# Optimization experiments

Hardware: AMD Instinct MI355X
Metric: run time of the kernel (lower is better)

## Reference

```python
import jax, jax.numpy as jnp
import numpy as np


def setup_inputs() -> dict:
    key = jax.random.key(0)
    k1, k2 = jax.random.split(key)
    B, S, D, T = 64, 1024, 512, 2048
    x = jax.random.normal(k1, (B, S, D), dtype=jnp.float32)
    durations = jax.random.randint(k2, (B, S), 0, 8, dtype=jnp.int32)
    return {"x": x, "durations": durations, "max_length": T}


def reference(x, durations, max_length):
    # x: [B, S, D]; durations: [B, S] (non-negative ints); max_length: static int.
    # Equivalent to per-sample repeat_interleave + pad_sequence + slice to max_length,
    # assuming max(sum(durations, axis=1)) >= max_length (true by construction here,
    # matching torch's min(lengths.max(), max_length) == max_length).
    S = x.shape[1]
    cum = jnp.cumsum(durations, axis=1)          # [B, S] exclusive boundary cumsum
    t = jnp.arange(max_length)                   # [T]
    # idx[b, t] = source phoneme index producing output frame t
    idx = jax.vmap(lambda c: jnp.searchsorted(c, t, side='right'))(cum)  # [B, T]
    lengths = cum[:, -1]                         # [B] total frames per sample
    mask = t[None, :] >= lengths[:, None]        # [B, T] True = padding (matches torch ~(<))
    idx = jnp.minimum(idx, S - 1)                # clip out-of-range indices (masked anyway)
    out = jnp.take_along_axis(x, idx[:, :, None], axis=1)  # [B, T, D] gather
    out = jnp.where(mask[:, :, None], jnp.zeros((), x.dtype), out)  # pad value 0
    return out, mask
```

## Files before the change

kernel.cpp:

```cpp
#include <hip/hip_runtime.h>

constexpr int B = 64;
constexpr int S = 1024;
constexpr int D = 512;
constexpr int T = 2048;
constexpr int FPB = 64;
constexpr int CHUNKS = T / FPB;

typedef float floatx4 __attribute__((ext_vector_type(4)));

__global__ __launch_bounds__(256) void lr_scan_kernel(
    const int* __restrict__ dur,
    int*       __restrict__ fidx,
    float*     __restrict__ mask)
{
    __shared__ int cum[S];
    __shared__ int wave_tot[4];

    const int tid  = threadIdx.x;
    const int b    = blockIdx.x;
    const int lane = tid & 63;
    const int wv   = tid >> 6;

    const int4 d4 = ((const int4*)(dur + b * S))[tid];
    const int p0 = d4.x;
    const int p1 = p0 + d4.y;
    const int p2 = p1 + d4.z;
    const int p3 = p2 + d4.w;

    int incl = p3;
    #pragma unroll
    for (int off = 1; off < 64; off <<= 1) {
        const int v = __shfl_up(incl, off, 64);
        if (lane >= off) incl += v;
    }
    if (lane == 63) wave_tot[wv] = incl;
    __syncthreads();
    int woff = 0;
    #pragma unroll
    for (int w = 0; w < 4; ++w) woff += (w < wv) ? wave_tot[w] : 0;

    const int excl = woff + incl - p3;
    cum[4 * tid + 0] = excl + p0;
    cum[4 * tid + 1] = excl + p1;
    cum[4 * tid + 2] = excl + p2;
    cum[4 * tid + 3] = excl + p3;
    __syncthreads();
    const int len = cum[S - 1];

    #pragma unroll
    for (int k = 0; k < T / 256; ++k) {
        const int t = k * 256 + tid;
        int id = -1;
        if (t < len) {
            int lo = 0, hi = S;
            while (lo < hi) {
                const int mid = (lo + hi) >> 1;
                if (cum[mid] > t) hi = mid; else lo = mid + 1;
            }
            id = lo;
        }
        fidx[b * T + t] = id;
        mask[b * T + t] = (id < 0) ? 1.0f : 0.0f;
    }
}

__global__ __launch_bounds__(256) void lr_copy_kernel(
    const float* __restrict__ x,
    const int*   __restrict__ fidx,
    float*       __restrict__ out)
{
    __shared__ int fr[FPB];

    const int tid   = threadIdx.x;
    const int chunk = blockIdx.x;
    const int b     = blockIdx.y;
    const int t0    = chunk * FPB;

    if (tid < FPB) fr[tid] = fidx[b * T + t0 + tid];
    __syncthreads();

    const int wv   = tid >> 6;
    const int lane = tid & 63;
    const floatx4* xb = (const floatx4*)(x + (size_t)b * S * D);
    floatx4*       ob = (floatx4*)(out + ((size_t)b * T + t0) * D)
                        + (size_t)(wv * 16) * (D / 4);

    int sid[16];
    #pragma unroll
    for (int k = 0; k < 16; ++k)
        sid[k] = __builtin_amdgcn_readfirstlane(fr[wv * 16 + k]);

    #pragma unroll
    for (int batch = 0; batch < 2; ++batch) {
        floatx4 v[8][2];
        #pragma unroll
        for (int f = 0; f < 8; ++f) {
            const int id = sid[batch * 8 + f];
            v[f][0] = (floatx4)(0.f);
            v[f][1] = (floatx4)(0.f);
            if (id >= 0) {
                const floatx4* src = xb + (size_t)id * (D / 4);
                v[f][0] = src[lane];
                v[f][1] = src[lane + 64];
            }
        }
        #pragma unroll
        for (int f = 0; f < 8; ++f) {
            floatx4* dst = ob + (size_t)(batch * 8 + f) * (D / 4);
            __builtin_nontemporal_store(v[f][0], dst + lane);
            __builtin_nontemporal_store(v[f][1], dst + lane + 64);
        }
    }
}

extern "C" void kernel_launch(void* const* d_in, const int* in_sizes, int n_in,
                              void* d_out, int out_size, void* d_ws, size_t ws_size,
                              hipStream_t stream) {
    const float* x   = (const float*)d_in[0];
    const int*   dur = (const int*)d_in[1];
    float* out  = (float*)d_out;
    float* mask = out + (size_t)B * T * D;
    int*   fidx = (int*)d_ws;

    lr_scan_kernel<<<B, 256, 0, stream>>>(dur, fidx, mask);
    dim3 grid(CHUNKS, B);
    lr_copy_kernel<<<grid, 256, 0, stream>>>(x, fidx, out);
}
```

Before: 355.1 us.

## Fuse duration scan into copy kernel with per-chunk scatter of frame indices

```diff
diff --git a/kernel.cpp b/kernel.cpp
--- a/kernel.cpp
+++ b/kernel.cpp
@@ -9,18 +9,24 @@
 
 typedef float floatx4 __attribute__((ext_vector_type(4)));
 
-__global__ __launch_bounds__(256) void lr_scan_kernel(
-    const int* __restrict__ dur,
-    int*       __restrict__ fidx,
-    float*     __restrict__ mask)
+__global__ __launch_bounds__(256) void lr_fused_kernel(
+    const float* __restrict__ x,
+    const int*   __restrict__ dur,
+    float*       __restrict__ out,
+    float*       __restrict__ mask)
 {
-    __shared__ int cum[S];
+    __shared__ int fr[FPB];
     __shared__ int wave_tot[4];
 
-    const int tid  = threadIdx.x;
-    const int b    = blockIdx.x;
-    const int lane = tid & 63;
-    const int wv   = tid >> 6;
+    const int tid   = threadIdx.x;
+    const int chunk = blockIdx.x;
+    const int b     = blockIdx.y;
+    const int t0    = chunk * FPB;
+    const int t1    = t0 + FPB;
+    const int lane  = tid & 63;
+    const int wv    = tid >> 6;
+
+    if (tid < FPB) fr[tid] = -1;
 
     const int4 d4 = ((const int4*)(dur + b * S))[tid];
     const int p0 = d4.x;
@@ -36,52 +42,31 @@
     }
     if (lane == 63) wave_tot[wv] = incl;
     __syncthreads();
+
     int woff = 0;
     #pragma unroll
     for (int w = 0; w < 4; ++w) woff += (w < wv) ? wave_tot[w] : 0;
+    const int excl = woff + incl - p3;
 
-    const int excl = woff + incl - p3;
-    cum[4 * tid + 0] = excl + p0;
-    cum[4 * tid + 1] = excl + p1;
-    cum[4 * tid + 2] = excl + p2;
-    cum[4 * tid + 3] = excl + p3;
-    __syncthreads();
-    const int len = cum[S - 1];
-
+    const int s0 = 4 * tid;
+    const int st0 = excl;
+    const int st1 = excl + p0;
+    const int st2 = excl + p1;
+    const int st3 = excl + p2;
+    const int st4 = excl + p3;
     #pragma unroll
-    for (int k = 0; k < T / 256; ++k) {
-        const int t = k * 256 + tid;
-        int id = -1;
-        if (t < len) {
-            int lo = 0, hi = S;
-            while (lo < hi) {
-                const int mid = (lo + hi) >> 1;
-                if (cum[mid] > t) hi = mid; else lo = mid + 1;
-            }
-            id = lo;
-        }
-        fidx[b * T + t] = id;
-        mask[b * T + t] = (id < 0) ? 1.0f : 0.0f;
+    for (int j = 0; j < 4; ++j) {
+        const int a0 = (j == 0) ? st0 : (j == 1) ? st1 : (j == 2) ? st2 : st3;
+        const int e0 = (j == 0) ? st1 : (j == 1) ? st2 : (j == 2) ? st3 : st4;
+        int a = a0 < t0 ? t0 : a0;
+        const int e = e0 > t1 ? t1 : e0;
+        for (int t = a; t < e; ++t) fr[t - t0] = s0 + j;
     }
-}
-
-__global__ __launch_bounds__(256) void lr_copy_kernel(
-    const float* __restrict__ x,
-    const int*   __restrict__ fidx,
-    float*       __restrict__ out)
-{
-    __shared__ int fr[FPB];
-
-    const int tid   = threadIdx.x;
-    const int chunk = blockIdx.x;
-    const int b     = blockIdx.y;
-    const int t0    = chunk * FPB;
-
-    if (tid < FPB) fr[tid] = fidx[b * T + t0 + tid];
     __syncthreads();
 
-    const int wv   = tid >> 6;
-    const int lane = tid & 63;
+    if (tid < FPB)
+        mask[(size_t)b * T + t0 + tid] = (fr[tid] < 0) ? 1.0f : 0.0f;
+
     const floatx4* xb = (const floatx4*)(x + (size_t)b * S * D);
     floatx4*       ob = (floatx4*)(out + ((size_t)b * T + t0) * D)
                         + (size_t)(wv * 16) * (D / 4);
@@ -121,9 +106,7 @@
     const int*   dur = (const int*)d_in[1];
     float* out  = (float*)d_out;
     float* mask = out + (size_t)B * T * D;
-    int*   fidx = (int*)d_ws;
 
-    lr_scan_kernel<<<B, 256, 0, stream>>>(dur, fidx, mask);
     dim3 grid(CHUNKS, B);
-    lr_copy_kernel<<<grid, 256, 0, stream>>>(x, fidx, out);
+    lr_fused_kernel<<<grid, 256, 0, stream>>>(x, dur, out, mask);
 }
```

Measured after the change: 347.5 us. -2.1%, faster.
